# Performance work log

Measured on AMD Instinct MI355X. Metric: run time of the kernel, lower is better.

The kernel has to match this reference:

```python
import jax, jax.numpy as jnp
import numpy as np

B, S, D, H = 4, 1024, 1024, 16
HD = D // H


def setup_inputs() -> dict:
    key = jax.random.key(0)
    ks = jax.random.split(key, 12)
    s = 1.0 / np.sqrt(D)
    inp = {
        'q': jax.random.normal(ks[0], (B, S, D), jnp.float32),
        'k': jax.random.normal(ks[1], (B, S, D), jnp.float32),
        'v': jax.random.normal(ks[2], (B, S, D), jnp.float32),
        'mask': jnp.broadcast_to(jnp.tril(jnp.ones((S, S), jnp.int32)), (B, S, S)),
        'Wq': jax.random.uniform(ks[3], (D, D), jnp.float32, -s, s),
        'bq': jax.random.uniform(ks[4], (D,), jnp.float32, -s, s),
        'Wk': jax.random.uniform(ks[5], (D, D), jnp.float32, -s, s),
        'bk': jax.random.uniform(ks[6], (D,), jnp.float32, -s, s),
        'Wv': jax.random.uniform(ks[7], (D, D), jnp.float32, -s, s),
        'bv': jax.random.uniform(ks[8], (D,), jnp.float32, -s, s),
        'Wo': jax.random.uniform(ks[9], (D, D), jnp.float32, -s, s),
        'bo': jax.random.uniform(ks[10], (D,), jnp.float32, -s, s),
    }
    return inp


def _split_heads(x):
    # [B,S,D] -> [B,H,S,HD]
    b, s, d = x.shape
    return x.reshape(b, s, H, HD).transpose(0, 2, 1, 3)


def reference(q, k, v, mask, Wq, bq, Wk, bk, Wv, bv, Wo, bo):
    # Linear projections (torch Linear: x @ W.T + b) followed by relu
    qh = jax.nn.relu(q @ Wq.T + bq)
    kh = jax.nn.relu(k @ Wk.T + bk)
    vh = jax.nn.relu(v @ Wv.T + bv)
    qh, kh, vh = _split_heads(qh), _split_heads(kh), _split_heads(vh)
    scores = jnp.einsum('bhqd,bhkd->bhqk', qh, kh) / jnp.sqrt(jnp.float32(HD))
    scores = jnp.where(mask[:, None, :, :] == 0, jnp.float32(-1e9), scores)
    attn = jax.nn.softmax(scores, axis=-1)
    y = jnp.einsum('bhqk,bhkd->bhqd', attn, vh)
    y = y.transpose(0, 2, 1, 3).reshape(B, S, D)  # merge heads
    return jax.nn.relu(y @ Wo.T + bo)
```

## Files before the change

kernel.cpp:

```cpp
#include <hip/hip_runtime.h>


using f16    = _Float16;
using f16x4  = __attribute__((ext_vector_type(4))) _Float16;
using f16x8  = __attribute__((ext_vector_type(8))) _Float16;
using f32x4  = __attribute__((ext_vector_type(4))) float;
using f32x16 = __attribute__((ext_vector_type(16))) float;

static constexpr int S = 1024, Dm = 1024, NH = 16, HD = 64;

#if __has_builtin(__builtin_amdgcn_mfma_f32_32x32x8f16)
#define USE_MFMA32 1
#define MFMA32(ACC, A_, B_) \
    (ACC) = __builtin_amdgcn_mfma_f32_32x32x8f16((A_), (B_), (ACC), 0, 0, 0)
#else
#define USE_MFMA32 0
#endif
#if __has_builtin(__builtin_amdgcn_mfma_f32_16x16x16f16)
#define USE_MFMA 1
#define MFMA16(ACC, A_, B_) \
    (ACC) = __builtin_amdgcn_mfma_f32_16x16x16f16((A_), (B_), (ACC), 0, 0, 0)
#else
#define USE_MFMA 0
#endif

#define LO4(v) __builtin_shufflevector((v), (v), 0, 1, 2, 3)
#define HI4(v) __builtin_shufflevector((v), (v), 4, 5, 6, 7)

__device__ __forceinline__ f16x4 cvt4(float4 a) {
    f16x4 r; r[0] = (f16)a.x; r[1] = (f16)a.y; r[2] = (f16)a.z; r[3] = (f16)a.w;
    return r;
}
__device__ __forceinline__ int pcol64(int k) {
    return ((k >> 2) & 3) * 16 + ((k >> 4) << 2) + (k & 3);
}

__device__ __forceinline__ void store_out(void* out, int mode, int m, int n, float v) {
    if (mode == 2) {
        ((float*)out)[(size_t)m * Dm + n] = v;
    } else {
        const int b_ = m >> 10, s_ = m & 1023, h_ = n >> 6, hd_ = n & 63;
        const size_t idx = (mode == 0)
            ? (((size_t)(b_ * NH + h_) * S + s_) * HD + pcol64(hd_))
            : (((size_t)(b_ * NH + h_) * HD + hd_) * S + s_);
        ((f16*)out)[idx] = (f16)v;
    }
}

template <int AF32>
__device__ __forceinline__ void gemm_core(const void* __restrict__ A,
                                          const float* __restrict__ W,
                                          const float* __restrict__ bias,
                                          void* __restrict__ out, int mode)
{
    const int tid = threadIdx.x;
    const int bm = blockIdx.x, bn = blockIdx.y;
#if USE_MFMA32
    __shared__ alignas(16) f16 As[2][128][36];
    __shared__ alignas(16) f16 Ws[2][128][36];

    const int lane = tid & 63, wave = tid >> 6;
    const int l31 = lane & 31, kh = lane >> 5;
    const int wm = wave & 1, wn = wave >> 1;

    const int ar = tid >> 3, ac = (tid & 7) * 4;
    const int ar2 = tid >> 2, ac2 = (tid & 3) * 8;
    const float* Af = (const float*)A + (size_t)(bm * 128 + ar) * Dm + ac;
    const f16*   Ah = (const f16*)A   + (size_t)(bm * 128 + ar2) * Dm + ac2;
    const float* Wf = W + (size_t)(bn * 128 + ar) * Dm + ac;

    float4 pa[4]; uint4 pah[2]; float4 pw[4];
    auto pref = [&](int k0) {
        if (AF32) {
#pragma unroll
            for (int i = 0; i < 4; ++i) pa[i] = *(const float4*)(Af + k0 + (size_t)i * 32 * Dm);
        } else {
#pragma unroll
            for (int i = 0; i < 2; ++i) pah[i] = *(const uint4*)(Ah + k0 + (size_t)i * 64 * Dm);
        }
#pragma unroll
        for (int i = 0; i < 4; ++i) pw[i] = *(const float4*)(Wf + k0 + (size_t)i * 32 * Dm);
    };
    auto stage = [&](int cur) {
        if (AF32) {
#pragma unroll
            for (int i = 0; i < 4; ++i) *(f16x4*)&As[cur][ar + i * 32][ac] = cvt4(pa[i]);
        } else {
#pragma unroll
            for (int i = 0; i < 2; ++i) *(f16x8*)&As[cur][ar2 + i * 64][ac2] = *(f16x8*)&pah[i];
        }
#pragma unroll
        for (int i = 0; i < 4; ++i) *(f16x4*)&Ws[cur][ar + i * 32][ac] = cvt4(pw[i]);
    };

    f32x16 acc[2][2] = {};
    pref(0);
    for (int it = 0; it < Dm / 32; ++it) {
        const int cur = it & 1;
        stage(cur);
        __syncthreads();
        if (it < Dm / 32 - 1) pref((it + 1) * 32);

#pragma unroll
        for (int s = 0; s < 4; ++s) {
            f16x4 af[2], bf[2];
            const int c = s * 8 + kh * 4;
            af[0] = *(const f16x4*)&As[cur][wm * 64 + l31][c];
            af[1] = *(const f16x4*)&As[cur][wm * 64 + 32 + l31][c];
            bf[0] = *(const f16x4*)&Ws[cur][wn * 64 + l31][c];
            bf[1] = *(const f16x4*)&Ws[cur][wn * 64 + 32 + l31][c];
            MFMA32(acc[0][0], af[0], bf[0]);
            MFMA32(acc[0][1], af[0], bf[1]);
            MFMA32(acc[1][0], af[1], bf[0]);
            MFMA32(acc[1][1], af[1], bf[1]);
        }
    }

#pragma unroll
    for (int g2 = 0; g2 < 2; ++g2) {
        const int col = bn * 128 + wn * 64 + g2 * 32 + l31;
        const float bb = bias[col];
#pragma unroll
        for (int g = 0; g < 2; ++g)
#pragma unroll
            for (int blk = 0; blk < 4; ++blk) {
                const int row0 = bm * 128 + wm * 64 + g * 32 + 8 * blk + 4 * kh;
                if (mode == 1) {
                    const int b_ = row0 >> 10, s_ = row0 & 1023;
                    const int h_ = col >> 6, hd_ = col & 63;
                    f16x4 v;
#pragma unroll
                    for (int r = 0; r < 4; ++r)
                        v[r] = (f16)fmaxf(acc[g][g2][blk * 4 + r] + bb, 0.0f);
                    *(f16x4*)&((f16*)out)[((size_t)(b_ * NH + h_) * HD + hd_) * S + s_] = v;
                } else {
#pragma unroll
                    for (int r = 0; r < 4; ++r)
                        store_out(out, mode, row0 + r, col,
                                  fmaxf(acc[g][g2][blk * 4 + r] + bb, 0.0f));
                }
            }
    }
#else
    for (int i = tid; i < 128 * 128; i += 256) {
        const int m = bm * 128 + (i >> 7);
        const int n = bn * 128 + (i & 127);
        float acc = 0.0f;
        for (int k = 0; k < Dm; ++k) {
            const float a = AF32 ? ((const float*)A)[(size_t)m * Dm + k]
                                 : (float)((const f16*)A)[(size_t)m * Dm + k];
            acc = fmaf(a, W[(size_t)n * Dm + k], acc);
        }
        store_out(out, mode, m, n, fmaxf(acc + bias[n], 0.0f));
    }
#endif
}

__global__ __launch_bounds__(256)
void gemm_qkv(const float* __restrict__ q, const float* __restrict__ k,
              const float* __restrict__ v,
              const float* __restrict__ Wq, const float* __restrict__ Wk,
              const float* __restrict__ Wv,
              const float* __restrict__ bq, const float* __restrict__ bk,
              const float* __restrict__ bv,
              f16* __restrict__ qh, f16* __restrict__ kh, f16* __restrict__ vt)
{
    const int z = blockIdx.z;
    const float* A = (z == 0) ? q : (z == 1) ? k : v;
    const float* W = (z == 0) ? Wq : (z == 1) ? Wk : Wv;
    const float* B = (z == 0) ? bq : (z == 1) ? bk : bv;
    f16* O = (z == 0) ? qh : (z == 1) ? kh : vt;
    gemm_core<1>(A, W, B, O, (z == 2) ? 1 : 0);
}

__global__ __launch_bounds__(256)
void gemm_out(const f16* __restrict__ y, const float* __restrict__ Wo,
              const float* __restrict__ bo, float* __restrict__ out)
{
    gemm_core<0>(y, Wo, bo, out, 2);
}

__global__ __launch_bounds__(256)
void attn_fwd(const f16* __restrict__ qh, const f16* __restrict__ kh,
              const f16* __restrict__ vt, f16* __restrict__ y)
{
    const int bz = blockIdx.x;
    const int qt = bz & 15;
    const int h  = (bz >> 4) & 15;
    const int b  = bz >> 8;
    const size_t head = (size_t)(b * NH + h) * S * HD;

#if USE_MFMA
    __shared__ alignas(16) f16 Ks[2][64][72];
    __shared__ alignas(16) f16 Vs[2][64][72];

    const int tid  = threadIdx.x;
    const int wave = tid >> 6;
    const int lane = tid & 63;
    const int l15  = lane & 15;
    const int quad = lane >> 4;
    const int sr   = tid >> 2;
    const int sc   = (tid & 3) * 16;

    const f16* Qrow = qh + head + (size_t)(qt * 64 + wave * 16 + l15) * HD;
    const f16* Kp   = kh + head;
    const f16* Vp   = vt + head;

    f16x4 aq[4];
    {
        const uint4 q0 = *(const uint4*)(Qrow + quad * 16);
        const uint4 q1 = *(const uint4*)(Qrow + quad * 16 + 8);
        aq[0] = *(f16x4*)((f16*)&q0);
        aq[1] = *(f16x4*)((f16*)&q0 + 4);
        aq[2] = *(f16x4*)((f16*)&q1);
        aq[3] = *(f16x4*)((f16*)&q1 + 4);
    }

    const int qg = qt * 64 + wave * 16 + l15;
    float m_i = -1e30f, l_i = 0.0f;
    f32x4 acc_o[4] = {};

    uint4 pk[2], pv[2];
    auto pref = [&](int kt) {
        const f16* Kr = Kp + (size_t)(kt * 64 + sr) * HD + sc;
        pk[0] = *(const uint4*)Kr;
        pk[1] = *(const uint4*)(Kr + 8);
        const f16* Vr = Vp + (size_t)sr * S + kt * 64 + sc;
        pv[0] = *(const uint4*)Vr;
        pv[1] = *(const uint4*)(Vr + 8);
    };

    pref(0);
    for (int kt = 0; kt <= qt; ++kt) {
        const int cur = kt & 1;
        *(uint4*)&Ks[cur][sr][sc]     = pk[0];
        *(uint4*)&Ks[cur][sr][sc + 8] = pk[1];
        {
            const int sb = (sc >> 4) * 4;
            *(f16x4*)&Vs[cur][sr][0 * 16 + sb] = *(f16x4*)((f16*)&pv[0]);
            *(f16x4*)&Vs[cur][sr][1 * 16 + sb] = *(f16x4*)((f16*)&pv[0] + 4);
            *(f16x4*)&Vs[cur][sr][2 * 16 + sb] = *(f16x4*)((f16*)&pv[1]);
            *(f16x4*)&Vs[cur][sr][3 * 16 + sb] = *(f16x4*)((f16*)&pv[1] + 4);
        }
        __syncthreads();
        if (kt < qt) pref(kt + 1);

        f32x4 accs[4] = {};
#pragma unroll
        for (int t = 0; t < 4; ++t) {
            const f16x8 k8a = *(const f16x8*)&Ks[cur][t * 16 + l15][quad * 16];
            const f16x8 k8b = *(const f16x8*)&Ks[cur][t * 16 + l15][quad * 16 + 8];
            MFMA16(accs[t], LO4(k8a), aq[0]);
            MFMA16(accs[t], HI4(k8a), aq[1]);
            MFMA16(accs[t], LO4(k8b), aq[2]);
            MFMA16(accs[t], HI4(k8b), aq[3]);
        }

        const int key0 = kt * 64 + quad * 4;
#pragma unroll
        for (int t = 0; t < 4; ++t)
#pragma unroll
            for (int r = 0; r < 4; ++r) {
                float sv = accs[t][r] * 0.125f;
                if (key0 + t * 16 + r > qg) sv = -1e9f;
                accs[t][r] = sv;
            }

        float mx = accs[0][0];
#pragma unroll
        for (int t = 0; t < 4; ++t)
#pragma unroll
            for (int r = 0; r < 4; ++r) mx = fmaxf(mx, accs[t][r]);
        mx = fmaxf(mx, __shfl_xor(mx, 16, 64));
        mx = fmaxf(mx, __shfl_xor(mx, 32, 64));
        const float mnew = fmaxf(m_i, mx);
        float sm = 0.0f;
#pragma unroll
        for (int t = 0; t < 4; ++t)
#pragma unroll
            for (int r = 0; r < 4; ++r) {
                const float e = __expf(accs[t][r] - mnew);
                accs[t][r] = e;
                sm += e;
            }
        sm += __shfl_xor(sm, 16, 64);
        sm += __shfl_xor(sm, 32, 64);
        const float alpha = __expf(m_i - mnew);
        l_i = l_i * alpha + sm;
        m_i = mnew;

        f16x4 ap[4];
#pragma unroll
        for (int c = 0; c < 4; ++c) {
            f16x4 v;
#pragma unroll
            for (int j = 0; j < 4; ++j) v[j] = (f16)accs[c][j];
            ap[c] = v;
        }

        float ar[4];
#pragma unroll
        for (int r = 0; r < 4; ++r) ar[r] = __shfl(alpha, quad * 4 + r, 64);
#pragma unroll
        for (int t2 = 0; t2 < 4; ++t2)
#pragma unroll
            for (int r = 0; r < 4; ++r) acc_o[t2][r] *= ar[r];
#pragma unroll
        for (int t2 = 0; t2 < 4; ++t2) {
            const f16x8 v8a = *(const f16x8*)&Vs[cur][t2 * 16 + l15][quad * 16];
            const f16x8 v8b = *(const f16x8*)&Vs[cur][t2 * 16 + l15][quad * 16 + 8];
            MFMA16(acc_o[t2], ap[0], LO4(v8a));
            MFMA16(acc_o[t2], ap[1], HI4(v8a));
            MFMA16(acc_o[t2], ap[2], LO4(v8b));
            MFMA16(acc_o[t2], ap[3], HI4(v8b));
        }
    }

    float lr[4];
#pragma unroll
    for (int r = 0; r < 4; ++r) lr[r] = __shfl(l_i, quad * 4 + r, 64);
#pragma unroll
    for (int t2 = 0; t2 < 4; ++t2)
#pragma unroll
        for (int r = 0; r < 4; ++r) {
            const int srow = qt * 64 + wave * 16 + quad * 4 + r;
            const int dcol = h * 64 + t2 * 16 + l15;
            y[((size_t)b * S + srow) * Dm + dcol] = (f16)(acc_o[t2][r] / lr[r]);
        }
#else
    const int tid = threadIdx.x;
    if (tid < 64) {
        const int q = qt * 64 + tid;
        const f16* Qr = qh + head + (size_t)q * HD;
        float qv[64];
        for (int d = 0; d < 64; ++d) qv[d] = (float)Qr[d];
        float mx = -1e30f;
        for (int key = 0; key <= q; ++key) {
            const f16* Kr = kh + head + (size_t)key * HD;
            float s = 0.0f;
            for (int d = 0; d < 64; ++d) s = fmaf(qv[d], (float)Kr[d], s);
            mx = fmaxf(mx, s * 0.125f);
        }
        float o[64];
        for (int d = 0; d < 64; ++d) o[d] = 0.0f;
        float l = 0.0f;
        for (int key = 0; key <= q; ++key) {
            const f16* Kr = kh + head + (size_t)key * HD;
            float s = 0.0f;
            for (int d = 0; d < 64; ++d) s = fmaf(qv[d], (float)Kr[d], s);
            const float p = __expf(s * 0.125f - mx);
            l += p;
            for (int d = 0; d < 64; ++d)
                o[d] = fmaf(p, (float)vt[head + (size_t)d * S + key], o[d]);
        }
        for (int d = 0; d < 64; ++d)
            y[((size_t)b * S + q) * Dm + h * 64 + d] = (f16)(o[d] / l);
    }
#endif
}

extern "C" void kernel_launch(void* const* d_in, const int* in_sizes, int n_in,
                              void* d_out, int out_size, void* d_ws, size_t ws_size,
                              hipStream_t stream)
{
    f16* ws = (f16*)d_ws;
    const size_t SEG = (size_t)4 * 1024 * 1024;
    f16* qh = ws;
    f16* kh = ws + SEG;
    f16* vt = ws + 2 * SEG;
    f16* y  = ws + 3 * SEG;

    gemm_qkv<<<dim3(32, 8, 3), 256, 0, stream>>>(
        (const float*)d_in[0], (const float*)d_in[1], (const float*)d_in[2],
        (const float*)d_in[4], (const float*)d_in[6], (const float*)d_in[8],
        (const float*)d_in[5], (const float*)d_in[7], (const float*)d_in[9],
        qh, kh, vt);
    attn_fwd<<<dim3(4 * NH * (S / 64)), 256, 0, stream>>>(qh, kh, vt, y);
    gemm_out<<<dim3(32, 8), 256, 0, stream>>>(
        y, (const float*)d_in[10], (const float*)d_in[11], (float*)d_out);
}
```

Before: 278.9 us.

## Pre-convert weights to swizzled f16, DMA tiles to LDS, use K=16/32 MFMAs

Adds a conversion kernel that turns the fp32 weights into f16 with an XOR-swizzled column layout, written into reused workspace. The GEMMs then load W tiles (and the f16 y activations in the output GEMM) straight into LDS with global_load_lds instead of going through registers with fp32 conversion. The GEMMs switch to the 32x32x16 MFMA and attention QK^T to the 16x16x32 MFMA, and the Q/K column permutation and y layout are changed to match. The goal is less global traffic and fewer instructions in the GEMM main loop, at the cost of two extra launches and a round trip through workspace for the converted weights.

New measurement: 264.0 us. 5.3% less time.

```diff
diff --git a/kernel.cpp b/kernel.cpp
--- a/kernel.cpp
+++ b/kernel.cpp
@@ -9,19 +9,23 @@
 
 static constexpr int S = 1024, Dm = 1024, NH = 16, HD = 64;
 
-#if __has_builtin(__builtin_amdgcn_mfma_f32_32x32x8f16)
-#define USE_MFMA32 1
+#if __has_builtin(__builtin_amdgcn_mfma_f32_32x32x16_f16)
+#define USE_G32 1
 #define MFMA32(ACC, A_, B_) \
-    (ACC) = __builtin_amdgcn_mfma_f32_32x32x8f16((A_), (B_), (ACC), 0, 0, 0)
-#else
-#define USE_MFMA32 0
-#endif
-#if __has_builtin(__builtin_amdgcn_mfma_f32_16x16x16f16)
-#define USE_MFMA 1
+    (ACC) = __builtin_amdgcn_mfma_f32_32x32x16_f16((A_), (B_), (ACC), 0, 0, 0)
+#else
+#define USE_G32 0
+#endif
+
+#if __has_builtin(__builtin_amdgcn_mfma_f32_16x16x32_f16) && \
+    __has_builtin(__builtin_amdgcn_mfma_f32_16x16x16f16)
+#define USE_A16 1
+#define MFMA16K32(ACC, A_, B_) \
+    (ACC) = __builtin_amdgcn_mfma_f32_16x16x32_f16((A_), (B_), (ACC), 0, 0, 0)
 #define MFMA16(ACC, A_, B_) \
     (ACC) = __builtin_amdgcn_mfma_f32_16x16x16f16((A_), (B_), (ACC), 0, 0, 0)
 #else
-#define USE_MFMA 0
+#define USE_A16 0
 #endif
 
 #define LO4(v) __builtin_shufflevector((v), (v), 0, 1, 2, 3)
@@ -31,8 +35,17 @@
     f16x4 r; r[0] = (f16)a.x; r[1] = (f16)a.y; r[2] = (f16)a.z; r[3] = (f16)a.w;
     return r;
 }
+
 __device__ __forceinline__ int pcol64(int k) {
+#if USE_A16
+    return ((k >> 3) & 3) * 16 + ((k >> 5) << 3) + (k & 7);
+#else
     return ((k >> 2) & 3) * 16 + ((k >> 4) << 2) + (k & 3);
+#endif
+}
+
+__device__ __forceinline__ int swz(int row, int col) {
+    return (col & ~31) | ((((col >> 3) ^ row) & 3) << 3) | (col & 7);
 }
 
 __device__ __forceinline__ void store_out(void* out, int mode, int m, int n, float v) {
@@ -47,68 +60,107 @@
     }
 }
 
-template <int AF32>
+#if __has_builtin(__builtin_amdgcn_global_load_lds)
+#define HAS_GLL 1
+#else
+#define HAS_GLL 0
+#endif
+
+__device__ __forceinline__ void gll16(const f16* g, f16* l) {
+#if HAS_GLL
+    __builtin_amdgcn_global_load_lds(
+        (const __attribute__((address_space(1))) void*)g,
+        (__attribute__((address_space(3))) void*)l, 16, 0, 0);
+#else
+    *(uint4*)l = *(const uint4*)g;
+#endif
+}
+
+__global__ __launch_bounds__(256)
+void cvt_w(const float* __restrict__ s0, const float* __restrict__ s1,
+           const float* __restrict__ s2, f16* __restrict__ dst)
+{
+    const int z = blockIdx.y;
+    const float* src = (z == 0) ? s0 : (z == 1) ? s1 : s2;
+    const int e = blockIdx.x * 256 + threadIdx.x;
+    const int n = e >> 8;
+    const int k = (e & 255) * 4;
+    const float4 v = *(const float4*)(src + (size_t)n * Dm + k);
+    *(f16x4*)(dst + (size_t)z * Dm * Dm + (size_t)n * Dm + swz(n, k)) = cvt4(v);
+}
+
+template <int ADMA>
 __device__ __forceinline__ void gemm_core(const void* __restrict__ A,
-                                          const float* __restrict__ W,
+                                          const f16* __restrict__ Wf,
                                           const float* __restrict__ bias,
                                           void* __restrict__ out, int mode)
 {
     const int tid = threadIdx.x;
     const int bm = blockIdx.x, bn = blockIdx.y;
-#if USE_MFMA32
-    __shared__ alignas(16) f16 As[2][128][36];
-    __shared__ alignas(16) f16 Ws[2][128][36];
+#if USE_G32
+    __shared__ alignas(16) f16 As[2][128][ADMA ? 32 : 36];
+    __shared__ alignas(16) f16 Ws[2][128][32];
 
     const int lane = tid & 63, wave = tid >> 6;
     const int l31 = lane & 31, kh = lane >> 5;
     const int wm = wave & 1, wn = wave >> 1;
 
+    const int dr = wave * 16 + (lane >> 2);
+    const int dc = (lane & 3) * 8;
+    const f16* Wsrc = Wf + (size_t)(bn * 128 + dr) * Dm + dc;
+    const f16* Asrc = (const f16*)A + (size_t)(bm * 128 + dr) * Dm + dc;
+
     const int ar = tid >> 3, ac = (tid & 7) * 4;
-    const int ar2 = tid >> 2, ac2 = (tid & 3) * 8;
     const float* Af = (const float*)A + (size_t)(bm * 128 + ar) * Dm + ac;
-    const f16*   Ah = (const f16*)A   + (size_t)(bm * 128 + ar2) * Dm + ac2;
-    const float* Wf = W + (size_t)(bn * 128 + ar) * Dm + ac;
-
-    float4 pa[4]; uint4 pah[2]; float4 pw[4];
-    auto pref = [&](int k0) {
-        if (AF32) {
-#pragma unroll
-            for (int i = 0; i < 4; ++i) pa[i] = *(const float4*)(Af + k0 + (size_t)i * 32 * Dm);
-        } else {
-#pragma unroll
-            for (int i = 0; i < 2; ++i) pah[i] = *(const uint4*)(Ah + k0 + (size_t)i * 64 * Dm);
-        }
-#pragma unroll
-        for (int i = 0; i < 4; ++i) pw[i] = *(const float4*)(Wf + k0 + (size_t)i * 32 * Dm);
+
+    float4 pa[4];
+    auto prefA = [&](int k0) {
+#pragma unroll
+        for (int i = 0; i < 4; ++i) pa[i] = *(const float4*)(Af + k0 + (size_t)i * 32 * Dm);
     };
-    auto stage = [&](int cur) {
-        if (AF32) {
-#pragma unroll
-            for (int i = 0; i < 4; ++i) *(f16x4*)&As[cur][ar + i * 32][ac] = cvt4(pa[i]);
-        } else {
-#pragma unroll
-            for (int i = 0; i < 2; ++i) *(f16x8*)&As[cur][ar2 + i * 64][ac2] = *(f16x8*)&pah[i];
-        }
-#pragma unroll
-        for (int i = 0; i < 4; ++i) *(f16x4*)&Ws[cur][ar + i * 32][ac] = cvt4(pw[i]);
+    auto stageA = [&](int cur) {
+#pragma unroll
+        for (int i = 0; i < 4; ++i) *(f16x4*)&As[cur][ar + i * 32][ac] = cvt4(pa[i]);
     };
+    auto dma = [&](int k0, int cur) {
+        gll16(Wsrc + k0, &Ws[cur][dr][dc]);
+        gll16(Wsrc + k0 + (size_t)64 * Dm, &Ws[cur][64 + dr][dc]);
+        if (ADMA) {
+            gll16(Asrc + k0, &As[cur][dr][dc]);
+            gll16(Asrc + k0 + (size_t)64 * Dm, &As[cur][64 + dr][dc]);
+        }
+    };
 
     f32x16 acc[2][2] = {};
-    pref(0);
+    if (!ADMA) prefA(0);
+    dma(0, 0);
     for (int it = 0; it < Dm / 32; ++it) {
         const int cur = it & 1;
-        stage(cur);
+        if (!ADMA) stageA(cur);
         __syncthreads();
-        if (it < Dm / 32 - 1) pref((it + 1) * 32);
-
-#pragma unroll
-        for (int s = 0; s < 4; ++s) {
-            f16x4 af[2], bf[2];
-            const int c = s * 8 + kh * 4;
-            af[0] = *(const f16x4*)&As[cur][wm * 64 + l31][c];
-            af[1] = *(const f16x4*)&As[cur][wm * 64 + 32 + l31][c];
-            bf[0] = *(const f16x4*)&Ws[cur][wn * 64 + l31][c];
-            bf[1] = *(const f16x4*)&Ws[cur][wn * 64 + 32 + l31][c];
+        if (it < Dm / 32 - 1) {
+            if (!ADMA) prefA((it + 1) * 32);
+            dma((it + 1) * 32, cur ^ 1);
+        }
+
+#pragma unroll
+        for (int s2 = 0; s2 < 2; ++s2) {
+            const int sl = s2 * 2 + kh;
+            f16x8 af[2], bf[2];
+#pragma unroll
+            for (int g = 0; g < 2; ++g) {
+                const int rr = g * 32 + l31;
+                const int slot = (sl ^ rr) & 3;
+                if (ADMA) {
+                    af[g] = *(const f16x8*)&As[cur][wm * 64 + rr][slot * 8];
+                } else {
+                    const int c = s2 * 16 + kh * 8;
+                    const f16x4 lo = *(const f16x4*)&As[cur][wm * 64 + rr][c];
+                    const f16x4 hi = *(const f16x4*)&As[cur][wm * 64 + rr][c + 4];
+                    af[g] = __builtin_shufflevector(lo, hi, 0, 1, 2, 3, 4, 5, 6, 7);
+                }
+                bf[g] = *(const f16x8*)&Ws[cur][wn * 64 + rr][slot * 8];
+            }
             MFMA32(acc[0][0], af[0], bf[0]);
             MFMA32(acc[0][1], af[0], bf[1]);
             MFMA32(acc[1][0], af[1], bf[0]);
@@ -128,11 +180,11 @@
                 if (mode == 1) {
                     const int b_ = row0 >> 10, s_ = row0 & 1023;
                     const int h_ = col >> 6, hd_ = col & 63;
-                    f16x4 v;
+                    f16x4 vv;
 #pragma unroll
                     for (int r = 0; r < 4; ++r)
-                        v[r] = (f16)fmaxf(acc[g][g2][blk * 4 + r] + bb, 0.0f);
-                    *(f16x4*)&((f16*)out)[((size_t)(b_ * NH + h_) * HD + hd_) * S + s_] = v;
+                        vv[r] = (f16)fmaxf(acc[g][g2][blk * 4 + r] + bb, 0.0f);
+                    *(f16x4*)&((f16*)out)[((size_t)(b_ * NH + h_) * HD + hd_) * S + s_] = vv;
                 } else {
 #pragma unroll
                     for (int r = 0; r < 4; ++r)
@@ -146,10 +198,10 @@
         const int m = bm * 128 + (i >> 7);
         const int n = bn * 128 + (i & 127);
         float acc = 0.0f;
-        for (int k = 0; k < Dm; ++k) {
-            const float a = AF32 ? ((const float*)A)[(size_t)m * Dm + k]
-                                 : (float)((const f16*)A)[(size_t)m * Dm + k];
-            acc = fmaf(a, W[(size_t)n * Dm + k], acc);
+        for (int k2 = 0; k2 < Dm; ++k2) {
+            const float a = ADMA ? (float)((const f16*)A)[(size_t)m * Dm + swz(m, k2)]
+                                 : ((const float*)A)[(size_t)m * Dm + k2];
+            acc = fmaf(a, (float)Wf[(size_t)n * Dm + swz(n, k2)], acc);
         }
         store_out(out, mode, m, n, fmaxf(acc + bias[n], 0.0f));
     }
@@ -158,26 +210,23 @@
 
 __global__ __launch_bounds__(256)
 void gemm_qkv(const float* __restrict__ q, const float* __restrict__ k,
-              const float* __restrict__ v,
-              const float* __restrict__ Wq, const float* __restrict__ Wk,
-              const float* __restrict__ Wv,
+              const float* __restrict__ v, const f16* __restrict__ wqkv,
               const float* __restrict__ bq, const float* __restrict__ bk,
               const float* __restrict__ bv,
               f16* __restrict__ qh, f16* __restrict__ kh, f16* __restrict__ vt)
 {
     const int z = blockIdx.z;
     const float* A = (z == 0) ? q : (z == 1) ? k : v;
-    const float* W = (z == 0) ? Wq : (z == 1) ? Wk : Wv;
     const float* B = (z == 0) ? bq : (z == 1) ? bk : bv;
     f16* O = (z == 0) ? qh : (z == 1) ? kh : vt;
-    gemm_core<1>(A, W, B, O, (z == 2) ? 1 : 0);
+    gemm_core<0>(A, wqkv + (size_t)z * Dm * Dm, B, O, (z == 2) ? 1 : 0);
 }
 
 __global__ __launch_bounds__(256)
-void gemm_out(const f16* __restrict__ y, const float* __restrict__ Wo,
+void gemm_out(const f16* __restrict__ y, const f16* __restrict__ wo,
               const float* __restrict__ bo, float* __restrict__ out)
 {
-    gemm_core<0>(y, Wo, bo, out, 2);
+    gemm_core<1>(y, wo, bo, out, 2);
 }
 
 __global__ __launch_bounds__(256)
@@ -190,7 +239,7 @@
     const int b  = bz >> 8;
     const size_t head = (size_t)(b * NH + h) * S * HD;
 
-#if USE_MFMA
+#if USE_A16
     __shared__ alignas(16) f16 Ks[2][64][72];
     __shared__ alignas(16) f16 Vs[2][64][72];
 
@@ -206,14 +255,12 @@
     const f16* Kp   = kh + head;
     const f16* Vp   = vt + head;
 
-    f16x4 aq[4];
+    f16x8 aq[2];
     {
         const uint4 q0 = *(const uint4*)(Qrow + quad * 16);
         const uint4 q1 = *(const uint4*)(Qrow + quad * 16 + 8);
-        aq[0] = *(f16x4*)((f16*)&q0);
-        aq[1] = *(f16x4*)((f16*)&q0 + 4);
-        aq[2] = *(f16x4*)((f16*)&q1);
-        aq[3] = *(f16x4*)((f16*)&q1 + 4);
+        aq[0] = *(f16x8*)&q0;
+        aq[1] = *(f16x8*)&q1;
     }
 
     const int qg = qt * 64 + wave * 16 + l15;
@@ -250,10 +297,8 @@
         for (int t = 0; t < 4; ++t) {
             const f16x8 k8a = *(const f16x8*)&Ks[cur][t * 16 + l15][quad * 16];
             const f16x8 k8b = *(const f16x8*)&Ks[cur][t * 16 + l15][quad * 16 + 8];
-            MFMA16(accs[t], LO4(k8a), aq[0]);
-            MFMA16(accs[t], HI4(k8a), aq[1]);
-            MFMA16(accs[t], LO4(k8b), aq[2]);
-            MFMA16(accs[t], HI4(k8b), aq[3]);
+            MFMA16K32(accs[t], k8a, aq[0]);
+            MFMA16K32(accs[t], k8b, aq[1]);
         }
 
         const int key0 = kt * 64 + quad * 4;
@@ -325,7 +370,8 @@
         for (int r = 0; r < 4; ++r) {
             const int srow = qt * 64 + wave * 16 + quad * 4 + r;
             const int dcol = h * 64 + t2 * 16 + l15;
-            y[((size_t)b * S + srow) * Dm + dcol] = (f16)(acc_o[t2][r] / lr[r]);
+            y[((size_t)b * S + srow) * Dm + swz(srow, dcol)] =
+                (f16)(acc_o[t2][r] / lr[r]);
         }
 #else
     const int tid = threadIdx.x;
@@ -333,12 +379,12 @@
         const int q = qt * 64 + tid;
         const f16* Qr = qh + head + (size_t)q * HD;
         float qv[64];
-        for (int d = 0; d < 64; ++d) qv[d] = (float)Qr[d];
+        for (int d = 0; d < 64; ++d) qv[d] = (float)Qr[pcol64(d)];
         float mx = -1e30f;
         for (int key = 0; key <= q; ++key) {
             const f16* Kr = kh + head + (size_t)key * HD;
             float s = 0.0f;
-            for (int d = 0; d < 64; ++d) s = fmaf(qv[d], (float)Kr[d], s);
+            for (int d = 0; d < 64; ++d) s = fmaf(qv[d], (float)Kr[pcol64(d)], s);
             mx = fmaxf(mx, s * 0.125f);
         }
         float o[64];
@@ -347,14 +393,14 @@
         for (int key = 0; key <= q; ++key) {
             const f16* Kr = kh + head + (size_t)key * HD;
             float s = 0.0f;
-            for (int d = 0; d < 64; ++d) s = fmaf(qv[d], (float)Kr[d], s);
+            for (int d = 0; d < 64; ++d) s = fmaf(qv[d], (float)Kr[pcol64(d)], s);
             const float p = __expf(s * 0.125f - mx);
             l += p;
             for (int d = 0; d < 64; ++d)
                 o[d] = fmaf(p, (float)vt[head + (size_t)d * S + key], o[d]);
         }
         for (int d = 0; d < 64; ++d)
-            y[((size_t)b * S + q) * Dm + h * 64 + d] = (f16)(o[d] / l);
+            y[((size_t)b * S + q) * Dm + swz(q, h * 64 + d)] = (f16)(o[d] / l);
     }
 #endif
 }
@@ -365,17 +411,23 @@
 {
     f16* ws = (f16*)d_ws;
     const size_t SEG = (size_t)4 * 1024 * 1024;
-    f16* qh = ws;
-    f16* kh = ws + SEG;
-    f16* vt = ws + 2 * SEG;
-    f16* y  = ws + 3 * SEG;
-
+    f16* qh   = ws;
+    f16* kh   = ws + SEG;
+    f16* vt   = ws + 2 * SEG;
+    f16* wqkv = ws + 3 * SEG;
+    f16* y    = ws + 3 * SEG;
+    f16* wo   = ws;
+
+    cvt_w<<<dim3(1024, 3), 256, 0, stream>>>(
+        (const float*)d_in[4], (const float*)d_in[6], (const float*)d_in[8], wqkv);
     gemm_qkv<<<dim3(32, 8, 3), 256, 0, stream>>>(
         (const float*)d_in[0], (const float*)d_in[1], (const float*)d_in[2],
-        (const float*)d_in[4], (const float*)d_in[6], (const float*)d_in[8],
+        wqkv,
         (const float*)d_in[5], (const float*)d_in[7], (const float*)d_in[9],
         qh, kh, vt);
     attn_fwd<<<dim3(4 * NH * (S / 64)), 256, 0, stream>>>(qh, kh, vt, y);
+    cvt_w<<<dim3(1024, 1), 256, 0, stream>>>(
+        (const float*)d_in[10], nullptr, nullptr, wo);
     gemm_out<<<dim3(32, 8), 256, 0, stream>>>(
-        y, (const float*)d_in[10], (const float*)d_in[11], (float*)d_out);
-}
+        y, wo, (const float*)d_in[11], (float*)d_out);
+}
```
